# Kernel optimization log

Measured on AMD Instinct MI355X. Metric: run time of the kernel, lower is better.

## Reference

```python
import jax, jax.numpy as jnp
from jax import lax
import numpy as np

NPOINT, K, EPS = 2048, 16, 1e-5


def fps(xyz, npoint):
    # Farthest point sampling. Deterministic start index 0 (torch uses randint).
    B, N, _ = xyz.shape
    def step(carry, _):
        distance, far = carry
        centroid = jnp.take_along_axis(xyz, far[:, None, None], axis=1)  # [B,1,3]
        d = jnp.sum((xyz - centroid) ** 2, axis=-1)                      # [B,N]
        distance = jnp.minimum(distance, d)
        return (distance, jnp.argmax(distance, axis=-1)), far
    init = (jnp.full((B, N), 1e10, dtype=xyz.dtype), jnp.zeros((B,), jnp.int32))
    _, cent = lax.scan(step, init, None, length=npoint)  # [npoint, B]
    return jnp.transpose(cent)  # [B, npoint]


def gather(points, idx):
    # points [B,N,C], idx [B,...] -> [B,...,C]
    return jax.vmap(lambda p, i: p[i])(points, idx)


def bn_relu(x, gamma, beta):
    # x [B,S,K,C]; BatchNorm2d training-mode stats over (B,S,K) per channel
    mu = jnp.mean(x, axis=(0, 1, 2), keepdims=True)
    var = jnp.var(x, axis=(0, 1, 2), keepdims=True)
    return jax.nn.relu((x - mu) * lax.rsqrt(var + EPS) * gamma + beta)


def setup_inputs() -> dict:
    key = jax.random.key(0)
    ks = jax.random.split(key, 8)
    B, N, C_in, C_out = 4, 8192, 64, 128
    return {
        'xyz': jax.random.normal(ks[0], (B, N, 3), jnp.float32),
        'feat': jax.random.normal(ks[1], (B, N, C_in), jnp.float32),
        'W1': jax.random.normal(ks[2], (C_in + 3, C_out), jnp.float32) * 0.05,
        'g1': jnp.ones((C_out,), jnp.float32),
        'b1': jnp.zeros((C_out,), jnp.float32),
        'W2': jax.random.normal(ks[3], (C_out, C_out), jnp.float32) * 0.05,
        'g2': jnp.ones((C_out,), jnp.float32),
        'b2': jnp.zeros((C_out,), jnp.float32),
    }


def reference(xyz, feat, W1, g1, b1, W2, g2, b2):
    fps_idx = fps(xyz, NPOINT)
    new_xyz = gather(xyz, fps_idx)                              # [B,S,3]
    # squared distances [B,S,N] via ||a||^2 + ||b||^2 - 2 a.b (avoids [B,S,N,3])
    d = (jnp.sum(new_xyz ** 2, -1)[:, :, None]
         + jnp.sum(xyz ** 2, -1)[:, None, :]
         - 2.0 * jnp.einsum('bsc,bnc->bsn', new_xyz, xyz))
    _, idx = lax.top_k(-d, K)                                   # [B,S,K] smallest dists
    g_xyz = gather(xyz, idx)                                    # [B,S,K,3]
    g_feat = gather(feat, idx)                                  # [B,S,K,C]
    x = jnp.concatenate([g_feat, g_xyz - new_xyz[:, :, None]], axis=-1)
    x = bn_relu(jnp.einsum('bskc,co->bsko', x, W1), g1, b1)     # 1x1 conv == matmul
    x = bn_relu(jnp.einsum('bskc,co->bsko', x, W2), g2, b2)
    new_feat = jnp.max(x, axis=2)                               # max over K -> [B,S,Cout]
    return new_xyz, new_feat
```

## Files before the change

kernel.cpp:

```cpp
#include <hip/hip_runtime.h>
#include <hip/hip_bf16.h>

#define N_PTS 8192
#define N_SAMP 2048
#define KNN_K 16
#define NBATCH 4
#define BN_M (NBATCH * N_SAMP * KNN_K)
#define NROWS (N_SAMP * NBATCH * KNN_K)
#define KNN_WAVES 2016
#define CHUNK 128

typedef float f32x2 __attribute__((ext_vector_type(2)));

template <int CTRL, int RM>
__device__ __forceinline__ unsigned umax_dpp(unsigned v) {
  unsigned o = (unsigned)__builtin_amdgcn_update_dpp((int)v, (int)v, CTRL, RM, 0xF, false);
  return (o > v) ? o : v;
}

__global__ __launch_bounds__(512) void fused_fps_knn(
    const float* __restrict__ xyz, float* __restrict__ new_xyz,
    int* __restrict__ knn_idx, int* __restrict__ progress) {
#pragma clang fp contract(off)
  __shared__ __align__(16) float xyzw[N_PTS * 4];
  __shared__ unsigned redbuf[8];
  __shared__ unsigned winslot[2];
  __shared__ int sampwin[CHUNK];
  const int tid = threadIdx.x;
  const int lane = tid & 63;

  if (blockIdx.x < NBATCH) {
    const int b = blockIdx.x;
    const int wid = tid >> 6;
    const float* base = xyz + (size_t)b * N_PTS * 3;
    for (int i = tid; i < N_PTS * 3; i += 512) {
      float v = base[i];
      int p = i / 3, c = i - p * 3;
      xyzw[p * 4 + c] = v;
    }
    for (int i = tid; i < N_PTS; i += 512) xyzw[i * 4 + 3] = 0.f;
    if (tid == 0) { winslot[0] = 0u; winslot[1] = 0xFFFFFFFFu; }
    __syncthreads();

    f32x2 px[8], py[8], pz[8], dmin[8];
#pragma unroll
    for (int j = 0; j < 8; ++j) {
      int p0 = (2 * j) * 512 + tid, p1 = p0 + 512;
      const float4 a = *reinterpret_cast<const float4*>(&xyzw[p0 * 4]);
      const float4 c = *reinterpret_cast<const float4*>(&xyzw[p1 * 4]);
      px[j] = f32x2{a.x, c.x};
      py[j] = f32x2{a.y, c.y};
      pz[j] = f32x2{a.z, c.z};
      dmin[j] = f32x2{1e10f, 1e10f};
    }
    for (int it = 1; it < N_SAMP; ++it) {
      const int p = it & 1;
      const unsigned cur = winslot[p ^ 1];
      if (tid == 0) sampwin[(it - 1) & (CHUNK - 1)] = (int)cur;
      const bool pub = (it & (CHUNK - 1)) == 0;
      if (pub && tid < CHUNK) {
        const int idx = (tid == CHUNK - 1) ? (int)cur : sampwin[tid];
        const float4 c4 = *reinterpret_cast<const float4*>(&xyzw[idx * 4]);
        float* dst = new_xyz + ((size_t)b * N_SAMP + (it - CHUNK) + tid) * 3;
        dst[0] = c4.x; dst[1] = c4.y; dst[2] = c4.z;
      }
      const float4 c4 = *reinterpret_cast<const float4*>(&xyzw[cur * 4]);
      f32x2 cX = {c4.x, c4.x}, cY = {c4.y, c4.y}, cZ = {c4.z, c4.z};
#pragma unroll
      for (int j = 0; j < 8; ++j) {
        f32x2 dx = px[j] - cX;
        f32x2 dy = py[j] - cY;
        f32x2 dz = pz[j] - cZ;
        f32x2 s01 = dx * dx + dy * dy;
        f32x2 d = s01 + dz * dz;
        dmin[j].x = fminf(dmin[j].x, d.x);
        dmin[j].y = fminf(dmin[j].y, d.y);
      }
      f32x2 m0 = {fmaxf(dmin[0].x, dmin[1].x), fmaxf(dmin[0].y, dmin[1].y)};
      f32x2 m1 = {fmaxf(dmin[2].x, dmin[3].x), fmaxf(dmin[2].y, dmin[3].y)};
      f32x2 m2 = {fmaxf(dmin[4].x, dmin[5].x), fmaxf(dmin[4].y, dmin[5].y)};
      f32x2 m3 = {fmaxf(dmin[6].x, dmin[7].x), fmaxf(dmin[6].y, dmin[7].y)};
      f32x2 n0 = {fmaxf(m0.x, m1.x), fmaxf(m0.y, m1.y)};
      f32x2 n1 = {fmaxf(m2.x, m3.x), fmaxf(m2.y, m3.y)};
      f32x2 nn = {fmaxf(n0.x, n1.x), fmaxf(n0.y, n1.y)};
      const unsigned bd = __float_as_uint(fmaxf(nn.x, nn.y));
      unsigned r = bd;
      r = umax_dpp<0xB1, 0xF>(r);
      r = umax_dpp<0x4E, 0xF>(r);
      r = umax_dpp<0x124, 0xF>(r);
      r = umax_dpp<0x128, 0xF>(r);
      r = umax_dpp<0x142, 0xA>(r);
      r = umax_dpp<0x143, 0xC>(r);
      if (lane == 63) redbuf[wid] = r;
      __syncthreads();
      if (tid == 0) {
        winslot[p ^ 1] = 0xFFFFFFFFu;
        if (pub)
          __hip_atomic_store(&progress[b], it, __ATOMIC_RELEASE, __HIP_MEMORY_SCOPE_AGENT);
      }
      unsigned g = redbuf[lane & 7];
      g = umax_dpp<0xB1, 0xF>(g);
      g = umax_dpp<0x4E, 0xF>(g);
      g = umax_dpp<0x124, 0xF>(g);
      if (bd == g) {
        unsigned cand = 0xFFFFFFFFu;
#pragma unroll
        for (int j = 7; j >= 0; --j) {
          if (__float_as_uint(dmin[j].y) == g) cand = (unsigned)((2 * j + 1) * 512 + tid);
          if (__float_as_uint(dmin[j].x) == g) cand = (unsigned)((2 * j) * 512 + tid);
        }
        atomicMin(&winslot[p], cand);
      }
      __syncthreads();
    }
    {
      const unsigned last = winslot[(N_SAMP - 1) & 1];
      if (tid < CHUNK) {
        const int idx = (tid == CHUNK - 1) ? (int)last : sampwin[tid];
        const float4 c4 = *reinterpret_cast<const float4*>(&xyzw[idx * 4]);
        float* dst = new_xyz + ((size_t)b * N_SAMP + (N_SAMP - CHUNK) + tid) * 3;
        dst[0] = c4.x; dst[1] = c4.y; dst[2] = c4.z;
      }
      __syncthreads();
      if (tid == 0)
        __hip_atomic_store(&progress[b], N_SAMP, __ATOMIC_RELEASE, __HIP_MEMORY_SCOPE_AGENT);
    }
  } else {
    const int wv = (int)(blockIdx.x - NBATCH) * 8 + (tid >> 6);
    for (int q4 = wv; q4 < NBATCH * N_SAMP; q4 += KNN_WAVES) {
      const int b = q4 & 3, s = q4 >> 2;
      while (__hip_atomic_load(&progress[b], __ATOMIC_RELAXED, __HIP_MEMORY_SCOPE_AGENT) <= s)
        __builtin_amdgcn_s_sleep(64);
      (void)__hip_atomic_load(&progress[b], __ATOMIC_ACQUIRE, __HIP_MEMORY_SCOPE_AGENT);
      const int q = b * N_SAMP + s;
      const float* qp = new_xyz + (size_t)q * 3;
      float q0 = qp[0], q1 = qp[1], q2 = qp[2];
      float qn = __fadd_rn(__fadd_rn(__fmul_rn(q0, q0), __fmul_rn(q1, q1)), __fmul_rn(q2, q2));
      const float* pb = xyz + (size_t)b * N_PTS * 3;
      unsigned long long arr[16];
#pragma unroll
      for (int i = 0; i < 16; ++i) arr[i] = ~0ull;
      for (int p = lane; p < N_PTS; p += 64) {
        float p0 = pb[p * 3 + 0], p1 = pb[p * 3 + 1], p2 = pb[p * 3 + 2];
        float pn = __fadd_rn(__fadd_rn(__fmul_rn(p0, p0), __fmul_rn(p1, p1)), __fmul_rn(p2, p2));
        float dt = fmaf(q2, p2, fmaf(q1, p1, __fmul_rn(q0, p0)));
        float d = __fsub_rn(__fadd_rn(qn, pn), __fmul_rn(2.0f, dt));
        unsigned ub = __float_as_uint(d);
        ub ^= (unsigned)((int)ub >> 31) | 0x80000000u;
        unsigned long long key = ((unsigned long long)ub << 32) | (unsigned)p;
        if (key < arr[15]) {
          unsigned long long curk = key;
#pragma unroll
          for (int j = 0; j < 16; ++j) {
            unsigned long long lo = (curk < arr[j]) ? curk : arr[j];
            unsigned long long hi = (curk < arr[j]) ? arr[j] : curk;
            arr[j] = lo; curk = hi;
          }
        }
      }
      for (int r = 0; r < KNN_K; ++r) {
        unsigned long long m = arr[0];
#pragma unroll
        for (int o = 32; o > 0; o >>= 1) {
          unsigned long long other = __shfl_xor(m, o, 64);
          m = (other < m) ? other : m;
        }
        if (arr[0] == m) {
#pragma unroll
          for (int j = 0; j < 15; ++j) arr[j] = arr[j + 1];
          arr[15] = ~0ull;
        }
        if (lane == r) knn_idx[(size_t)q * KNN_K + r] = (int)(m & 0xFFFFFFFFu);
      }
    }
  }
}

__global__ __launch_bounds__(256) void gemm1_kernel(
    const float* __restrict__ xyz, const float* __restrict__ feat,
    const float* __restrict__ W1, const float* __restrict__ new_xyz,
    const int* __restrict__ knn_i, float* __restrict__ y1, float* __restrict__ stats1) {
  __shared__ __align__(16) float At[67 * 128];
  __shared__ __align__(16) float Wq[17 * 128];
  __shared__ float part[4 * 256];
  __shared__ int nb[128];
  const int t = threadIdx.x, blk = blockIdx.x;
  const int row0 = blk * 128;
  if (t < 128) nb[t] = knn_i[row0 + t];
  __syncthreads();
  {
    const int r = t >> 1, q = t & 1;
    const int rg = row0 + r, bs = rg >> 4, b = bs >> 11;
    const float* fr = feat + ((size_t)b * N_PTS + nb[r]) * 64 + q * 32;
#pragma unroll
    for (int i = 0; i < 8; ++i) {
      float4 v = *reinterpret_cast<const float4*>(fr + 4 * i);
      int c = q * 32 + 4 * i;
      At[(c + 0) * 128 + r] = v.x; At[(c + 1) * 128 + r] = v.y;
      At[(c + 2) * 128 + r] = v.z; At[(c + 3) * 128 + r] = v.w;
    }
    if (q == 0) {
      const float* pr = xyz + ((size_t)b * N_PTS + nb[r]) * 3;
      const float* qr = new_xyz + (size_t)bs * 3;
      At[64 * 128 + r] = pr[0] - qr[0];
      At[65 * 128 + r] = pr[1] - qr[1];
      At[66 * 128 + r] = pr[2] - qr[2];
    }
  }
  float acc[8][8];
#pragma unroll
  for (int i = 0; i < 8; ++i)
#pragma unroll
    for (int j = 0; j < 8; ++j) acc[i][j] = 0.f;
  const int ry = t >> 4, cx = t & 15;
  for (int kq = 0; kq < 4; ++kq) {
    const int kbase = kq * 17;
    const int nk = (67 - kbase) < 17 ? (67 - kbase) : 17;
    __syncthreads();
    for (int i = t; i < nk * 32; i += 256)
      reinterpret_cast<float4*>(Wq)[i] =
          reinterpret_cast<const float4*>(W1 + (size_t)kbase * 128)[i];
    __syncthreads();
    for (int kk = 0; kk < nk; ++kk) {
      const float4 a0 = *reinterpret_cast<const float4*>(&At[(kbase + kk) * 128 + ry * 8]);
      const float4 a1 = *reinterpret_cast<const float4*>(&At[(kbase + kk) * 128 + ry * 8 + 4]);
      const float4 w0 = *reinterpret_cast<const float4*>(&Wq[kk * 128 + cx * 8]);
      const float4 w1 = *reinterpret_cast<const float4*>(&Wq[kk * 128 + cx * 8 + 4]);
      const float a[8] = {a0.x, a0.y, a0.z, a0.w, a1.x, a1.y, a1.z, a1.w};
      const float w[8] = {w0.x, w0.y, w0.z, w0.w, w1.x, w1.y, w1.z, w1.w};
#pragma unroll
      for (int i = 0; i < 8; ++i)
#pragma unroll
        for (int j = 0; j < 8; ++j) acc[i][j] = fmaf(a[i], w[j], acc[i][j]);
    }
  }
#pragma unroll
  for (int i = 0; i < 8; ++i) {
    float4 v0 = {acc[i][0], acc[i][1], acc[i][2], acc[i][3]};
    float4 v1 = {acc[i][4], acc[i][5], acc[i][6], acc[i][7]};
    float* dst = y1 + ((size_t)row0 + ry * 8 + i) * 128 + cx * 8;
    *reinterpret_cast<float4*>(dst) = v0;
    *reinterpret_cast<float4*>(dst + 4) = v1;
  }
  float s8[8], q8[8];
#pragma unroll
  for (int j = 0; j < 8; ++j) {
    s8[j] = 0.f; q8[j] = 0.f;
#pragma unroll
    for (int i = 0; i < 8; ++i) { s8[j] += acc[i][j]; q8[j] += acc[i][j] * acc[i][j]; }
  }
#pragma unroll
  for (int j = 0; j < 8; ++j) {
    s8[j] += __shfl_xor(s8[j], 16, 64); q8[j] += __shfl_xor(q8[j], 16, 64);
    s8[j] += __shfl_xor(s8[j], 32, 64); q8[j] += __shfl_xor(q8[j], 32, 64);
  }
  const int w = t >> 6, lane = t & 63;
  if (lane < 16) {
#pragma unroll
    for (int j = 0; j < 8; ++j) {
      part[w * 256 + lane * 8 + j] = s8[j];
      part[w * 256 + 128 + lane * 8 + j] = q8[j];
    }
  }
  __syncthreads();
  {
    int ch = t & 127, which = t >> 7;
    float v = part[0 * 256 + which * 128 + ch] + part[1 * 256 + which * 128 + ch] +
              part[2 * 256 + which * 128 + ch] + part[3 * 256 + which * 128 + ch];
    atomicAdd(&stats1[which * 128 + ch], v);
  }
}

__global__ __launch_bounds__(256) void gemm2_kernel(
    const float* __restrict__ y1, const float* __restrict__ W2,
    const float* __restrict__ stats1, const float* __restrict__ g1v,
    const float* __restrict__ b1v, float* __restrict__ ymax, float* __restrict__ ymin,
    float* __restrict__ stats2) {
  __shared__ __align__(16) float Ah[64 * 128];
  __shared__ __align__(16) float Wq[32 * 128];
  __shared__ float part[4 * 256];
  __shared__ float s1[128], h1[128];
  const int t = threadIdx.x, blk = blockIdx.x;
  const int row0 = blk * 128;
  const float inv_m = 1.0f / (float)BN_M;
  if (t < 128) {
    float m = stats1[t] * inv_m;
    float var = stats1[128 + t] * inv_m - m * m;
    float rs = rsqrtf(var + 1e-5f);
    float sc = rs * g1v[t];
    s1[t] = sc;
    h1[t] = b1v[t] - m * sc;
  }
  float acc[8][8];
#pragma unroll
  for (int i = 0; i < 8; ++i)
#pragma unroll
    for (int j = 0; j < 8; ++j) acc[i][j] = 0.f;
  const int ry = t >> 4, cx = t & 15;
  for (int kh = 0; kh < 2; ++kh) {
    __syncthreads();
    {
      const int r = t >> 1, q = t & 1;
      const float* src = y1 + ((size_t)row0 + r) * 128 + kh * 64 + q * 32;
#pragma unroll
      for (int i = 0; i < 8; ++i) {
        float4 v = *reinterpret_cast<const float4*>(src + 4 * i);
        int c = kh * 64 + q * 32 + 4 * i;
        int cl = c - kh * 64;
        Ah[(cl + 0) * 128 + r] = fmaxf(fmaf(v.x, s1[c + 0], h1[c + 0]), 0.f);
        Ah[(cl + 1) * 128 + r] = fmaxf(fmaf(v.y, s1[c + 1], h1[c + 1]), 0.f);
        Ah[(cl + 2) * 128 + r] = fmaxf(fmaf(v.z, s1[c + 2], h1[c + 2]), 0.f);
        Ah[(cl + 3) * 128 + r] = fmaxf(fmaf(v.w, s1[c + 3], h1[c + 3]), 0.f);
      }
    }
    for (int kq = 0; kq < 2; ++kq) {
      __syncthreads();
      const int kbase = kh * 64 + kq * 32;
      for (int i = t; i < 32 * 32; i += 256)
        reinterpret_cast<float4*>(Wq)[i] =
            reinterpret_cast<const float4*>(W2 + (size_t)kbase * 128)[i];
      __syncthreads();
      for (int kk = 0; kk < 32; ++kk) {
        const int kl = kq * 32 + kk;
        const float4 a0 = *reinterpret_cast<const float4*>(&Ah[kl * 128 + ry * 8]);
        const float4 a1 = *reinterpret_cast<const float4*>(&Ah[kl * 128 + ry * 8 + 4]);
        const float4 w0 = *reinterpret_cast<const float4*>(&Wq[kk * 128 + cx * 8]);
        const float4 w1 = *reinterpret_cast<const float4*>(&Wq[kk * 128 + cx * 8 + 4]);
        const float a[8] = {a0.x, a0.y, a0.z, a0.w, a1.x, a1.y, a1.z, a1.w};
        const float w[8] = {w0.x, w0.y, w0.z, w0.w, w1.x, w1.y, w1.z, w1.w};
#pragma unroll
        for (int i = 0; i < 8; ++i)
#pragma unroll
          for (int j = 0; j < 8; ++j) acc[i][j] = fmaf(a[i], w[j], acc[i][j]);
      }
    }
  }
  float mx[8], mn[8];
#pragma unroll
  for (int j = 0; j < 8; ++j) { mx[j] = acc[0][j]; mn[j] = acc[0][j]; }
#pragma unroll
  for (int i = 1; i < 8; ++i)
#pragma unroll
    for (int j = 0; j < 8; ++j) {
      mx[j] = fmaxf(mx[j], acc[i][j]);
      mn[j] = fminf(mn[j], acc[i][j]);
    }
#pragma unroll
  for (int j = 0; j < 8; ++j) {
    mx[j] = fmaxf(mx[j], __shfl_xor(mx[j], 16, 64));
    mn[j] = fminf(mn[j], __shfl_xor(mn[j], 16, 64));
  }
  if ((ry & 1) == 0) {
    const int smp = blk * 8 + (ry >> 1);
    float4 a0 = {mx[0], mx[1], mx[2], mx[3]}, a1 = {mx[4], mx[5], mx[6], mx[7]};
    float4 b0 = {mn[0], mn[1], mn[2], mn[3]}, b1 = {mn[4], mn[5], mn[6], mn[7]};
    float* dm = ymax + (size_t)smp * 128 + cx * 8;
    *reinterpret_cast<float4*>(dm) = a0; *reinterpret_cast<float4*>(dm + 4) = a1;
    float* dn = ymin + (size_t)smp * 128 + cx * 8;
    *reinterpret_cast<float4*>(dn) = b0; *reinterpret_cast<float4*>(dn + 4) = b1;
  }
  float s8[8], q8[8];
#pragma unroll
  for (int j = 0; j < 8; ++j) {
    s8[j] = 0.f; q8[j] = 0.f;
#pragma unroll
    for (int i = 0; i < 8; ++i) { s8[j] += acc[i][j]; q8[j] += acc[i][j] * acc[i][j]; }
  }
#pragma unroll
  for (int j = 0; j < 8; ++j) {
    s8[j] += __shfl_xor(s8[j], 16, 64); q8[j] += __shfl_xor(q8[j], 16, 64);
    s8[j] += __shfl_xor(s8[j], 32, 64); q8[j] += __shfl_xor(q8[j], 32, 64);
  }
  const int w = t >> 6, lane = t & 63;
  if (lane < 16) {
#pragma unroll
    for (int j = 0; j < 8; ++j) {
      part[w * 256 + lane * 8 + j] = s8[j];
      part[w * 256 + 128 + lane * 8 + j] = q8[j];
    }
  }
  __syncthreads();
  {
    int ch = t & 127, which = t >> 7;
    float v = part[0 * 256 + which * 128 + ch] + part[1 * 256 + which * 128 + ch] +
              part[2 * 256 + which * 128 + ch] + part[3 * 256 + which * 128 + ch];
    atomicAdd(&stats2[which * 128 + ch], v);
  }
}

__global__ __launch_bounds__(256) void pool_kernel(
    const float* __restrict__ ymax, const float* __restrict__ ymin,
    const float* __restrict__ stats2, const float* __restrict__ g2v,
    const float* __restrict__ b2v, float* __restrict__ out_feat) {
  const int idx = blockIdx.x * 256 + threadIdx.x;
  const int ch = idx & 127;
  const float inv_m = 1.0f / (float)BN_M;
  float m = stats2[ch] * inv_m;
  float var = stats2[128 + ch] * inv_m - m * m;
  float rs = rsqrtf(var + 1e-5f);
  float sc = rs * g2v[ch];
  float h = b2v[ch] - m * sc;
  float v = (sc > 0.f) ? ymax[idx] : ymin[idx];
  out_feat[idx] = fmaxf(fmaf(v, sc, h), 0.f);
}

extern "C" void kernel_launch(void* const* d_in, const int* in_sizes, int n_in,
                              void* d_out, int out_size, void* d_ws, size_t ws_size,
                              hipStream_t stream) {
  const float* xyz  = (const float*)d_in[0];
  const float* feat = (const float*)d_in[1];
  const float* W1   = (const float*)d_in[2];
  const float* g1   = (const float*)d_in[3];
  const float* b1   = (const float*)d_in[4];
  const float* W2   = (const float*)d_in[5];
  const float* g2   = (const float*)d_in[6];
  const float* b2   = (const float*)d_in[7];
  float* out = (float*)d_out;
  float* new_xyz = out;
  float* out_feat = out + NBATCH * N_SAMP * 3;

  int* fps_i = (int*)d_ws;
  int* knn_i = fps_i + NBATCH * N_SAMP;
  float* stats1 = (float*)(knn_i + NROWS);
  float* stats2 = stats1 + 256;
  int* progress = (int*)(stats2 + 256);
  float* y1 = (float*)(progress + 64);
  float* ymax = y1 + (size_t)NROWS * 128;
  float* ymin = ymax + (size_t)NBATCH * N_SAMP * 128;

  hipMemsetAsync(stats1, 0, (256 + 256 + 64) * sizeof(float), stream);
  hipLaunchKernelGGL(fused_fps_knn, dim3(NBATCH + 252), dim3(512), 0, stream,
                     xyz, new_xyz, knn_i, progress);
  hipLaunchKernelGGL(gemm1_kernel, dim3(NROWS / 128), dim3(256), 0, stream,
                     xyz, feat, W1, new_xyz, knn_i, y1, stats1);
  hipLaunchKernelGGL(gemm2_kernel, dim3(NROWS / 128), dim3(256), 0, stream,
                     y1, W2, stats1, g1, b1, ymax, ymin, stats2);
  hipLaunchKernelGGL(pool_kernel, dim3(NBATCH * N_SAMP * 128 / 256), dim3(256), 0, stream,
                     ymax, ymin, stats2, g2, b2, out_feat);
}
```

Before: 2.039 ms.

## Fuse gemm1 into persistent FPS/KNN kernel with per-query readiness flags

Folds the first gathered GEMM and its BN statistics into the persistent FPS+KNN kernel. A third group of blocks waits on per-query flags set by the KNN waves, then processes each 128-row tile while FPS is still running. The progress counters are also padded to separate cache lines. This hides gemm1 behind the serial FPS critical path and removes a launch. The cost is fewer KNN blocks (126 instead of 252), extra spin-waiting, and shared-memory pressure from the split into two half-blocks.

```diff
diff --git a/kernel.cpp b/kernel.cpp
--- a/kernel.cpp
+++ b/kernel.cpp
@@ -7,7 +7,9 @@
 #define NBATCH 4
 #define BN_M (NBATCH * N_SAMP * KNN_K)
 #define NROWS (N_SAMP * NBATCH * KNN_K)
-#define KNN_WAVES 2016
+#define NKNNBLK 126
+#define KNN_WAVES (NKNNBLK * 8)
+#define NG1BLK 126
 #define CHUNK 128
 
 typedef float f32x2 __attribute__((ext_vector_type(2)));
@@ -19,18 +21,22 @@
 }
 
 __global__ __launch_bounds__(512) void fused_fps_knn(
-    const float* __restrict__ xyz, float* __restrict__ new_xyz,
-    int* __restrict__ knn_idx, int* __restrict__ progress) {
+    const float* __restrict__ xyz, const float* __restrict__ feat,
+    const float* __restrict__ W1, float* __restrict__ new_xyz,
+    int* __restrict__ knn_idx, int* __restrict__ progress,
+    int* __restrict__ qflag, float* __restrict__ y1, float* __restrict__ stats1) {
 #pragma clang fp contract(off)
-  __shared__ __align__(16) float xyzw[N_PTS * 4];
+  __shared__ __align__(16) float smem[32768];
   __shared__ unsigned redbuf[8];
   __shared__ unsigned winslot[2];
   __shared__ int sampwin[CHUNK];
+  const int bid = blockIdx.x;
   const int tid = threadIdx.x;
   const int lane = tid & 63;
 
-  if (blockIdx.x < NBATCH) {
-    const int b = blockIdx.x;
+  if (bid < NBATCH) {
+    float* xyzw = smem;
+    const int b = bid;
     const int wid = tid >> 6;
     const float* base = xyz + (size_t)b * N_PTS * 3;
     for (int i = tid; i < N_PTS * 3; i += 512) {
@@ -96,7 +102,7 @@
       if (tid == 0) {
         winslot[p ^ 1] = 0xFFFFFFFFu;
         if (pub)
-          __hip_atomic_store(&progress[b], it, __ATOMIC_RELEASE, __HIP_MEMORY_SCOPE_AGENT);
+          __hip_atomic_store(&progress[b * 64], it, __ATOMIC_RELEASE, __HIP_MEMORY_SCOPE_AGENT);
       }
       unsigned g = redbuf[lane & 7];
       g = umax_dpp<0xB1, 0xF>(g);
@@ -123,15 +129,15 @@
       }
       __syncthreads();
       if (tid == 0)
-        __hip_atomic_store(&progress[b], N_SAMP, __ATOMIC_RELEASE, __HIP_MEMORY_SCOPE_AGENT);
-    }
-  } else {
-    const int wv = (int)(blockIdx.x - NBATCH) * 8 + (tid >> 6);
+        __hip_atomic_store(&progress[b * 64], N_SAMP, __ATOMIC_RELEASE, __HIP_MEMORY_SCOPE_AGENT);
+    }
+  } else if (bid < NBATCH + NKNNBLK) {
+    const int wv = (bid - NBATCH) * 8 + (tid >> 6);
     for (int q4 = wv; q4 < NBATCH * N_SAMP; q4 += KNN_WAVES) {
       const int b = q4 & 3, s = q4 >> 2;
-      while (__hip_atomic_load(&progress[b], __ATOMIC_RELAXED, __HIP_MEMORY_SCOPE_AGENT) <= s)
+      while (__hip_atomic_load(&progress[b * 64], __ATOMIC_RELAXED, __HIP_MEMORY_SCOPE_AGENT) <= s)
         __builtin_amdgcn_s_sleep(64);
-      (void)__hip_atomic_load(&progress[b], __ATOMIC_ACQUIRE, __HIP_MEMORY_SCOPE_AGENT);
+      (void)__hip_atomic_load(&progress[b * 64], __ATOMIC_ACQUIRE, __HIP_MEMORY_SCOPE_AGENT);
       const int q = b * N_SAMP + s;
       const float* qp = new_xyz + (size_t)q * 3;
       float q0 = qp[0], q1 = qp[1], q2 = qp[2];
@@ -172,102 +178,112 @@
         }
         if (lane == r) knn_idx[(size_t)q * KNN_K + r] = (int)(m & 0xFFFFFFFFu);
       }
-    }
-  }
-}
-
-__global__ __launch_bounds__(256) void gemm1_kernel(
-    const float* __restrict__ xyz, const float* __restrict__ feat,
-    const float* __restrict__ W1, const float* __restrict__ new_xyz,
-    const int* __restrict__ knn_i, float* __restrict__ y1, float* __restrict__ stats1) {
-  __shared__ __align__(16) float At[67 * 128];
-  __shared__ __align__(16) float Wq[17 * 128];
-  __shared__ float part[4 * 256];
-  __shared__ int nb[128];
-  const int t = threadIdx.x, blk = blockIdx.x;
-  const int row0 = blk * 128;
-  if (t < 128) nb[t] = knn_i[row0 + t];
-  __syncthreads();
-  {
-    const int r = t >> 1, q = t & 1;
-    const int rg = row0 + r, bs = rg >> 4, b = bs >> 11;
-    const float* fr = feat + ((size_t)b * N_PTS + nb[r]) * 64 + q * 32;
-#pragma unroll
-    for (int i = 0; i < 8; ++i) {
-      float4 v = *reinterpret_cast<const float4*>(fr + 4 * i);
-      int c = q * 32 + 4 * i;
-      At[(c + 0) * 128 + r] = v.x; At[(c + 1) * 128 + r] = v.y;
-      At[(c + 2) * 128 + r] = v.z; At[(c + 3) * 128 + r] = v.w;
-    }
-    if (q == 0) {
-      const float* pr = xyz + ((size_t)b * N_PTS + nb[r]) * 3;
-      const float* qr = new_xyz + (size_t)bs * 3;
-      At[64 * 128 + r] = pr[0] - qr[0];
-      At[65 * 128 + r] = pr[1] - qr[1];
-      At[66 * 128 + r] = pr[2] - qr[2];
-    }
-  }
-  float acc[8][8];
-#pragma unroll
-  for (int i = 0; i < 8; ++i)
-#pragma unroll
-    for (int j = 0; j < 8; ++j) acc[i][j] = 0.f;
-  const int ry = t >> 4, cx = t & 15;
-  for (int kq = 0; kq < 4; ++kq) {
-    const int kbase = kq * 17;
-    const int nk = (67 - kbase) < 17 ? (67 - kbase) : 17;
-    __syncthreads();
-    for (int i = t; i < nk * 32; i += 256)
-      reinterpret_cast<float4*>(Wq)[i] =
-          reinterpret_cast<const float4*>(W1 + (size_t)kbase * 128)[i];
-    __syncthreads();
-    for (int kk = 0; kk < nk; ++kk) {
-      const float4 a0 = *reinterpret_cast<const float4*>(&At[(kbase + kk) * 128 + ry * 8]);
-      const float4 a1 = *reinterpret_cast<const float4*>(&At[(kbase + kk) * 128 + ry * 8 + 4]);
-      const float4 w0 = *reinterpret_cast<const float4*>(&Wq[kk * 128 + cx * 8]);
-      const float4 w1 = *reinterpret_cast<const float4*>(&Wq[kk * 128 + cx * 8 + 4]);
-      const float a[8] = {a0.x, a0.y, a0.z, a0.w, a1.x, a1.y, a1.z, a1.w};
-      const float w[8] = {w0.x, w0.y, w0.z, w0.w, w1.x, w1.y, w1.z, w1.w};
+      if (lane == 0)
+        __hip_atomic_store(&qflag[q], 1, __ATOMIC_RELEASE, __HIP_MEMORY_SCOPE_AGENT);
+    }
+  } else {
+    const int half = tid >> 8, t = tid & 255;
+    float* At = smem + half * 8576;
+    float* Wq = smem + 17152 + half * 2176;
+    float* part = smem + 21504 + half * 1024;
+    int* nb = reinterpret_cast<int*>(smem + 23552) + half * 128;
+    for (int pidx = bid - (NBATCH + NKNNBLK); pidx < 512; pidx += NG1BLK) {
+      const int tile = 2 * pidx + half;
+      const int row0 = tile * 128;
+      const int smp0 = tile * 8;
+      if (t == 0) {
+        for (int ss = 0; ss < 8; ++ss)
+          while (__hip_atomic_load(&qflag[smp0 + ss], __ATOMIC_RELAXED,
+                                   __HIP_MEMORY_SCOPE_AGENT) == 0)
+            __builtin_amdgcn_s_sleep(32);
+      }
+      __syncthreads();
+      (void)__hip_atomic_load(&qflag[smp0], __ATOMIC_ACQUIRE, __HIP_MEMORY_SCOPE_AGENT);
+      if (t < 128) nb[t] = knn_idx[row0 + t];
+      __syncthreads();
+      {
+        const int r = t >> 1, q = t & 1;
+        const int rg = row0 + r, bs = rg >> 4, b = bs >> 11;
+        const float* fr = feat + ((size_t)b * N_PTS + nb[r]) * 64 + q * 32;
+#pragma unroll
+        for (int i = 0; i < 8; ++i) {
+          float4 v = *reinterpret_cast<const float4*>(fr + 4 * i);
+          int c = q * 32 + 4 * i;
+          At[(c + 0) * 128 + r] = v.x; At[(c + 1) * 128 + r] = v.y;
+          At[(c + 2) * 128 + r] = v.z; At[(c + 3) * 128 + r] = v.w;
+        }
+        if (q == 0) {
+          const float* pr = xyz + ((size_t)b * N_PTS + nb[r]) * 3;
+          const float* qr = new_xyz + (size_t)bs * 3;
+          At[64 * 128 + r] = pr[0] - qr[0];
+          At[65 * 128 + r] = pr[1] - qr[1];
+          At[66 * 128 + r] = pr[2] - qr[2];
+        }
+      }
+      float acc[8][8];
 #pragma unroll
       for (int i = 0; i < 8; ++i)
 #pragma unroll
-        for (int j = 0; j < 8; ++j) acc[i][j] = fmaf(a[i], w[j], acc[i][j]);
-    }
-  }
-#pragma unroll
-  for (int i = 0; i < 8; ++i) {
-    float4 v0 = {acc[i][0], acc[i][1], acc[i][2], acc[i][3]};
-    float4 v1 = {acc[i][4], acc[i][5], acc[i][6], acc[i][7]};
-    float* dst = y1 + ((size_t)row0 + ry * 8 + i) * 128 + cx * 8;
-    *reinterpret_cast<float4*>(dst) = v0;
-    *reinterpret_cast<float4*>(dst + 4) = v1;
-  }
-  float s8[8], q8[8];
-#pragma unroll
-  for (int j = 0; j < 8; ++j) {
-    s8[j] = 0.f; q8[j] = 0.f;
-#pragma unroll
-    for (int i = 0; i < 8; ++i) { s8[j] += acc[i][j]; q8[j] += acc[i][j] * acc[i][j]; }
-  }
-#pragma unroll
-  for (int j = 0; j < 8; ++j) {
-    s8[j] += __shfl_xor(s8[j], 16, 64); q8[j] += __shfl_xor(q8[j], 16, 64);
-    s8[j] += __shfl_xor(s8[j], 32, 64); q8[j] += __shfl_xor(q8[j], 32, 64);
-  }
-  const int w = t >> 6, lane = t & 63;
-  if (lane < 16) {
-#pragma unroll
-    for (int j = 0; j < 8; ++j) {
-      part[w * 256 + lane * 8 + j] = s8[j];
-      part[w * 256 + 128 + lane * 8 + j] = q8[j];
-    }
-  }
-  __syncthreads();
-  {
-    int ch = t & 127, which = t >> 7;
-    float v = part[0 * 256 + which * 128 + ch] + part[1 * 256 + which * 128 + ch] +
-              part[2 * 256 + which * 128 + ch] + part[3 * 256 + which * 128 + ch];
-    atomicAdd(&stats1[which * 128 + ch], v);
+        for (int j = 0; j < 8; ++j) acc[i][j] = 0.f;
+      const int ry = t >> 4, cx = t & 15;
+      for (int kq = 0; kq < 4; ++kq) {
+        const int kbase = kq * 17;
+        const int nk = (67 - kbase) < 17 ? (67 - kbase) : 17;
+        __syncthreads();
+        for (int i = t; i < nk * 32; i += 256)
+          reinterpret_cast<float4*>(Wq)[i] =
+              reinterpret_cast<const float4*>(W1 + (size_t)kbase * 128)[i];
+        __syncthreads();
+        for (int kk = 0; kk < nk; ++kk) {
+          const float4 a0 = *reinterpret_cast<const float4*>(&At[(kbase + kk) * 128 + ry * 8]);
+          const float4 a1 = *reinterpret_cast<const float4*>(&At[(kbase + kk) * 128 + ry * 8 + 4]);
+          const float4 w0 = *reinterpret_cast<const float4*>(&Wq[kk * 128 + cx * 8]);
+          const float4 w1 = *reinterpret_cast<const float4*>(&Wq[kk * 128 + cx * 8 + 4]);
+          const float a[8] = {a0.x, a0.y, a0.z, a0.w, a1.x, a1.y, a1.z, a1.w};
+          const float w[8] = {w0.x, w0.y, w0.z, w0.w, w1.x, w1.y, w1.z, w1.w};
+#pragma unroll
+          for (int i = 0; i < 8; ++i)
+#pragma unroll
+            for (int j = 0; j < 8; ++j) acc[i][j] = fmaf(a[i], w[j], acc[i][j]);
+        }
+      }
+#pragma unroll
+      for (int i = 0; i < 8; ++i) {
+        float4 v0 = {acc[i][0], acc[i][1], acc[i][2], acc[i][3]};
+        float4 v1 = {acc[i][4], acc[i][5], acc[i][6], acc[i][7]};
+        float* dst = y1 + ((size_t)row0 + ry * 8 + i) * 128 + cx * 8;
+        *reinterpret_cast<float4*>(dst) = v0;
+        *reinterpret_cast<float4*>(dst + 4) = v1;
+      }
+      float s8[8], q8[8];
+#pragma unroll
+      for (int j = 0; j < 8; ++j) {
+        s8[j] = 0.f; q8[j] = 0.f;
+#pragma unroll
+        for (int i = 0; i < 8; ++i) { s8[j] += acc[i][j]; q8[j] += acc[i][j] * acc[i][j]; }
+      }
+#pragma unroll
+      for (int j = 0; j < 8; ++j) {
+        s8[j] += __shfl_xor(s8[j], 16, 64); q8[j] += __shfl_xor(q8[j], 16, 64);
+        s8[j] += __shfl_xor(s8[j], 32, 64); q8[j] += __shfl_xor(q8[j], 32, 64);
+      }
+      const int w = t >> 6, ln = t & 63;
+      if (ln < 16) {
+#pragma unroll
+        for (int j = 0; j < 8; ++j) {
+          part[w * 256 + ln * 8 + j] = s8[j];
+          part[w * 256 + 128 + ln * 8 + j] = q8[j];
+        }
+      }
+      __syncthreads();
+      {
+        int ch = t & 127, which = t >> 7;
+        float v = part[0 * 256 + which * 128 + ch] + part[1 * 256 + which * 128 + ch] +
+                  part[2 * 256 + which * 128 + ch] + part[3 * 256 + which * 128 + ch];
+        atomicAdd(&stats1[which * 128 + ch], v);
+      }
+      __syncthreads();
+    }
   }
 }
 
@@ -424,15 +440,14 @@
   float* stats1 = (float*)(knn_i + NROWS);
   float* stats2 = stats1 + 256;
   int* progress = (int*)(stats2 + 256);
-  float* y1 = (float*)(progress + 64);
+  int* qflag = progress + 256;
+  float* y1 = (float*)(qflag + 8192);
   float* ymax = y1 + (size_t)NROWS * 128;
   float* ymin = ymax + (size_t)NBATCH * N_SAMP * 128;
 
-  hipMemsetAsync(stats1, 0, (256 + 256 + 64) * sizeof(float), stream);
-  hipLaunchKernelGGL(fused_fps_knn, dim3(NBATCH + 252), dim3(512), 0, stream,
-                     xyz, new_xyz, knn_i, progress);
-  hipLaunchKernelGGL(gemm1_kernel, dim3(NROWS / 128), dim3(256), 0, stream,
-                     xyz, feat, W1, new_xyz, knn_i, y1, stats1);
+  hipMemsetAsync(stats1, 0, (256 + 256 + 256 + 8192) * sizeof(float), stream);
+  hipLaunchKernelGGL(fused_fps_knn, dim3(NBATCH + NKNNBLK + NG1BLK), dim3(512), 0, stream,
+                     xyz, feat, W1, new_xyz, knn_i, progress, qflag, y1, stats1);
   hipLaunchKernelGGL(gemm2_kernel, dim3(NROWS / 128), dim3(256), 0, stream,
                      y1, W2, stats1, g1, b1, ymax, ymin, stats2);
   hipLaunchKernelGGL(pool_kernel, dim3(NBATCH * N_SAMP * 128 / 256), dim3(256), 0, stream,
```

New measurement: 2.094 ms. 1.03x slower.
